# Kernel optimization log

Measured on AMD Instinct MI355X. Metric: run time of the kernel, lower is better.

The kernel has to match this reference:

```python
import jax, jax.numpy as jnp
import numpy as np
import math

N_HEAD = 32
ROPE_BASE = 10000.0


def _rope_headwise(x):
    # Faithful to the source bug: x is [B, H, S, D] and the rotary module uses
    # x.shape[1] (= H) as the "sequence length", so the angle depends on the
    # head index, broadcast over the true sequence axis.
    B, H, S, D = x.shape
    inv_freq = 1.0 / (ROPE_BASE ** (jnp.arange(0, D, 2, dtype=jnp.float32) / D))  # [D/2]
    t = jnp.arange(H, dtype=jnp.float32)                                          # [H]
    freqs = t[:, None] * inv_freq[None, :]                                        # [H, D/2]
    # emb = cat(freqs, freqs)[..., :D//2] == freqs, so cos/sin are just over freqs
    cos = jnp.cos(freqs)[None, :, None, :]   # [1, H, 1, D/2]
    sin = jnp.sin(freqs)[None, :, None, :]
    x1, x2 = x[..., : D // 2], x[..., D // 2 :]
    return jnp.concatenate([x1 * cos - x2 * sin, x1 * sin + x2 * cos], axis=-1)


def setup_inputs() -> dict:
    key = jax.random.key(0)
    ks = jax.random.split(key, 5)
    B, S, E = 2, 2048, 2048
    scale = 0.02
    return {
        "x": jax.random.normal(ks[0], (B, S, E), dtype=jnp.float32),
        "Wq": jax.random.normal(ks[1], (E, E), dtype=jnp.float32) * scale,
        "bq": jnp.zeros((E,), dtype=jnp.float32),
        "Wk": jax.random.normal(ks[2], (E, E), dtype=jnp.float32) * scale,
        "bk": jnp.zeros((E,), dtype=jnp.float32),
        "Wv": jax.random.normal(ks[3], (E, E), dtype=jnp.float32) * scale,
        "bv": jnp.zeros((E,), dtype=jnp.float32),
        "Wo": jax.random.normal(ks[4], (E, E), dtype=jnp.float32) * scale,
        "bo": jnp.zeros((E,), dtype=jnp.float32),
    }


def reference(x, Wq, bq, Wk, bk, Wv, bv, Wo, bo):
    B, S, E = x.shape
    H = N_HEAD
    D = E // H

    def split_heads(y):  # [B,S,E] -> [B,H,S,D]
        return y.reshape(B, S, H, D).transpose(0, 2, 1, 3)

    q = split_heads(x @ Wq + bq)
    k = split_heads(x @ Wk + bk)
    v = split_heads(x @ Wv + bv)

    q = _rope_headwise(q)
    k = _rope_headwise(k)

    scores = jnp.einsum("bhqd,bhkd->bhqk", q, k) / math.sqrt(D)  # [B,H,S,S]
    causal = jnp.triu(jnp.ones((S, S), dtype=bool), k=1)
    scores = jnp.where(causal[None, None], -jnp.inf, scores)
    attn = jax.nn.softmax(scores, axis=-1)
    out = jnp.einsum("bhqk,bhkd->bhqd", attn, v)                 # [B,H,S,D]
    out = out.transpose(0, 2, 1, 3).reshape(B, S, E)
    return out @ Wo + bo
```

## Files before the change

kernel.cpp:

```cpp
#include <hip/hip_runtime.h>
#include <hip/hip_bf16.h>

#define B_ 2
#define S_ 2048
#define E_ 2048
#define H_ 32
#define M_ (B_*S_)

typedef __bf16 bf16x8 __attribute__((ext_vector_type(8)));
typedef float  f32x4  __attribute__((ext_vector_type(4)));

__device__ __forceinline__ ushort f2bf(float f) {
    uint u = __float_as_uint(f);
    u += 0x7fffu + ((u >> 16) & 1u);
    return (ushort)(u >> 16);
}
__device__ __forceinline__ uint pack2bf(float a, float b) {
    __hip_bfloat162 h = __float22bfloat162_rn(make_float2(a, b));
    return *(uint*)&h;
}
__device__ __forceinline__ float bf2f(ushort h) {
    return __uint_as_float(((uint)h) << 16);
}
__device__ __forceinline__ f32x4 f4zero() {
    f32x4 z; z[0]=0.f; z[1]=0.f; z[2]=0.f; z[3]=0.f; return z;
}
__device__ __forceinline__ void async16(const ushort* g, ushort* l) {
    __builtin_amdgcn_global_load_lds((const __attribute__((address_space(1))) void*)g,
                                     (__attribute__((address_space(3))) void*)l, 16, 0, 0);
}

__global__ __launch_bounds__(256) void cast_x_kernel(const float* __restrict__ x,
                                                     ushort* __restrict__ xb) {
    int i = (blockIdx.x * 256 + threadIdx.x) * 4;
    float4 v = *(const float4*)(x + i);
    uint2 o;
    o.x = pack2bf(v.x, v.y);
    o.y = pack2bf(v.z, v.w);
    *(uint2*)(xb + i) = o;
}

__global__ __launch_bounds__(256) void wtrans_kernel(const float* __restrict__ W0, const float* __restrict__ W1,
                                                     const float* __restrict__ W2, const float* __restrict__ W3,
                                                     ushort* __restrict__ T0, ushort* __restrict__ T1,
                                                     ushort* __restrict__ T2, ushort* __restrict__ T3) {
    const float* W = (blockIdx.z==0)?W0:(blockIdx.z==1)?W1:(blockIdx.z==2)?W2:W3;
    ushort*      T = (blockIdx.z==0)?T0:(blockIdx.z==1)?T1:(blockIdx.z==2)?T2:T3;
    __shared__ float tile[64][65];
    const int k0 = blockIdx.y * 64, n0 = blockIdx.x * 64;
    const int rr = threadIdx.x >> 4;
    const int cc = (threadIdx.x & 15) * 4;
    #pragma unroll
    for (int p = 0; p < 4; ++p) {
        int r = p * 16 + rr;
        float4 v = *(const float4*)(W + (size_t)(k0 + r) * E_ + n0 + cc);
        tile[r][cc+0] = v.x; tile[r][cc+1] = v.y; tile[r][cc+2] = v.z; tile[r][cc+3] = v.w;
    }
    __syncthreads();
    #pragma unroll
    for (int p = 0; p < 4; ++p) {
        int rn = p * 16 + rr;
        uint2 o;
        o.x = pack2bf(tile[cc+0][rn], tile[cc+1][rn]);
        o.y = pack2bf(tile[cc+2][rn], tile[cc+3][rn]);
        *(uint2*)(T + (size_t)(n0 + rn) * E_ + k0 + cc) = o;
    }
}

__global__ __launch_bounds__(256) void vtrans_kernel(const ushort* __restrict__ vb,
                                                     ushort* __restrict__ vt) {
    __shared__ ushort tile[64][65];
    const int bh = blockIdx.y, b = bh >> 5, h = bh & 31;
    const int s0 = blockIdx.x * 64;
    int tx = threadIdx.x & 63, ty = threadIdx.x >> 6;
    #pragma unroll
    for (int it = 0; it < 16; ++it) {
        int r = it * 4 + ty;
        tile[r][tx] = vb[(size_t)(b * S_ + s0 + r) * E_ + h * 64 + tx];
    }
    __syncthreads();
    #pragma unroll
    for (int it = 0; it < 16; ++it) {
        int r = it * 4 + ty;
        vt[(size_t)(bh * 64 + r) * S_ + s0 + tx] = tile[tx][r];
    }
}

#define VMW4 asm volatile("s_waitcnt vmcnt(4)" ::: "memory")
#define VMW0 asm volatile("s_waitcnt vmcnt(0)" ::: "memory")
#define MEMB asm volatile("" ::: "memory")

#define STA_(bf, kt, h) { _Pragma("unroll") for (int it_ = 0; it_ < 2; ++it_) { \
    async16(A + (size_t)(m0 + it_*128 + (h)*64 + srow) * E_ + (kt)*64 + scg*8,  \
            &As[bf][(it_*128 + (h)*64 + wave*8) * 64]); } }

#define STB_(bf, kt, h) { _Pragma("unroll") for (int it_ = 0; it_ < 2; ++it_) { \
    int rih_ = it_*64 + srow;                                                   \
    int ldr_ = ((rih_ >> 5) << 6) + (h)*32 + (rih_ & 31);                       \
    int rwb_ = it_*64 + wave*8;                                                 \
    int wbs_ = ((rwb_ >> 5) << 6) + (h)*32 + (rwb_ & 31);                       \
    async16(Bt + (size_t)(n0 + ldr_) * E_ + (kt)*64 + scg*8,                    \
            &Bs[bf][wbs_ * 64]); } }

#define PHASE_(bf, mh, nh, LA, LB, STAGES) {                                    \
    if (LA) {                                                                   \
      _Pragma("unroll") for (int m_ = 0; m_ < 4; ++m_)                          \
        _Pragma("unroll") for (int k_ = 0; k_ < 2; ++k_) {                      \
          int row_ = wm*128 + ((mh)*4 + m_)*16 + l15;                           \
          pa[m_][k_] = *(const bf16x8*)(&As[bf][row_*64 + (((k_*4 + quad) ^ (row_ & 7)) << 3)]); } } \
    if (LB) {                                                                   \
      _Pragma("unroll") for (int n_ = 0; n_ < 2; ++n_)                          \
        _Pragma("unroll") for (int k_ = 0; k_ < 2; ++k_) {                      \
          int row_ = wn*64 + ((nh)*2 + n_)*16 + l15;                            \
          pb[n_][k_] = *(const bf16x8*)(&Bs[bf][row_*64 + (((k_*4 + quad) ^ (row_ & 7)) << 3)]); } } \
    STAGES;                                                                     \
    MEMB; __builtin_amdgcn_s_barrier();                                         \
    __builtin_amdgcn_s_setprio(1);                                              \
    _Pragma("unroll") for (int k_ = 0; k_ < 2; ++k_)                            \
      _Pragma("unroll") for (int m_ = 0; m_ < 4; ++m_)                          \
        _Pragma("unroll") for (int n_ = 0; n_ < 2; ++n_)                        \
          acc[(mh)*4+m_][(nh)*2+n_] = __builtin_amdgcn_mfma_f32_16x16x32_bf16(  \
              pa[m_][k_], pb[n_][k_], acc[(mh)*4+m_][(nh)*2+n_], 0, 0, 0);      \
    __builtin_amdgcn_s_setprio(0);                                              \
    asm volatile("s_waitcnt lgkmcnt(0)" ::: "memory");                          \
    __builtin_amdgcn_sched_barrier(0);                                          \
    MEMB; __builtin_amdgcn_s_barrier(); MEMB;                                   \
  }

template<bool OUTF32, bool DOROPE, int NZ>
__global__ __launch_bounds__(512, 2) void gemm256(const ushort* __restrict__ A,
        const ushort* __restrict__ Bt0, const ushort* __restrict__ Bt1, const ushort* __restrict__ Bt2,
        const float* __restrict__ bias0, const float* __restrict__ bias1, const float* __restrict__ bias2,
        void* __restrict__ C0, void* __restrict__ C1, void* __restrict__ C2) {
    const int bid = blockIdx.x;
    const int z   = bid % NZ;
    const int nb  = (bid / NZ) % (E_ / 256);
    const int mb  = bid / (NZ * (E_ / 256));

    const ushort* Bt  = (z==0)?Bt0:(z==1)?Bt1:Bt2;
    const float* bias = (z==0)?bias0:(z==1)?bias1:bias2;
    void* Cv          = (z==0)?C0:(z==1)?C1:C2;

    __shared__ ushort As[2][256 * 64];
    __shared__ ushort Bs[2][256 * 64];

    const int tid  = threadIdx.x;
    const int wave = tid >> 6, lane = tid & 63;
    const int quad = lane >> 4, l15 = lane & 15;
    const int wm = wave >> 2, wn = wave & 3;
    const int m0 = mb * 256, n0 = nb * 256;
    const int srow = tid >> 3;
    const int scg  = (tid & 7) ^ (srow & 7);

    f32x4 acc[8][4];
    #pragma unroll
    for (int i = 0; i < 8; ++i)
        #pragma unroll
        for (int j = 0; j < 4; ++j) acc[i][j] = f4zero();

    bf16x8 pa[4][2], pb[2][2];

    STA_(0, 0, 0); STA_(0, 0, 1); STB_(0, 0, 0); STB_(0, 0, 1);
    STA_(1, 1, 0); STB_(1, 1, 0);
    VMW4;
    MEMB; __builtin_amdgcn_s_barrier(); MEMB;

    #pragma unroll 1
    for (int i = 0; i < 15; ++i) {
        const int t1 = 2*i + 1, t2 = 2*i + 2, t3 = 2*i + 3;
        PHASE_(0, 0, 1, 1, 1, STB_(1, t1, 1));
        PHASE_(0, 0, 0, 0, 1, STA_(1, t1, 1));
        PHASE_(0, 1, 0, 1, 0, STA_(0, t2, 0));
        PHASE_(0, 1, 1, 0, 1, STB_(0, t2, 0); VMW4);
        PHASE_(1, 0, 1, 1, 1, STB_(0, t2, 1));
        PHASE_(1, 0, 0, 0, 1, STA_(0, t2, 1));
        PHASE_(1, 1, 0, 1, 0, STA_(1, t3, 0));
        PHASE_(1, 1, 1, 0, 1, STB_(1, t3, 0); VMW4);
    }
    PHASE_(0, 0, 1, 1, 1, STB_(1, 31, 1));
    PHASE_(0, 0, 0, 0, 1, STA_(1, 31, 1));
    PHASE_(0, 1, 0, 1, 0, {});
    PHASE_(0, 1, 1, 0, 1, VMW0);
    PHASE_(1, 0, 1, 1, 1, {});
    PHASE_(1, 0, 0, 0, 1, {});
    PHASE_(1, 1, 0, 1, 0, {});
    PHASE_(1, 1, 1, 0, 1, {});

    if (DOROPE && z != 2) {
        const float qsc = (z == 0) ? 0.125f * 1.44269504f : 1.0f;
        const int h = (n0 + wn * 64) >> 6;
        float sn[2], cs[2];
        #pragma unroll
        for (int nt = 0; nt < 2; ++nt) {
            int j = nt * 16 + l15;
            float ang = (float)h * __expf(-(float)j * 0.28782313662425575f);
            __sincosf(ang, &sn[nt], &cs[nt]);
        }
        ushort* C = (ushort*)Cv;
        #pragma unroll
        for (int f = 0; f < 8; ++f) {
            #pragma unroll
            for (int nt = 0; nt < 2; ++nt) {
                int col1 = n0 + wn * 64 + nt * 16 + l15;
                float b1 = bias[col1], b2 = bias[col1 + 32];
                #pragma unroll
                for (int r = 0; r < 4; ++r) {
                    int rowg = m0 + wm * 128 + f * 16 + quad * 4 + r;
                    float x1 = acc[f][nt][r] + b1;
                    float x2 = acc[f][nt + 2][r] + b2;
                    C[(size_t)rowg * E_ + col1]      = f2bf((x1 * cs[nt] - x2 * sn[nt]) * qsc);
                    C[(size_t)rowg * E_ + col1 + 32] = f2bf((x1 * sn[nt] + x2 * cs[nt]) * qsc);
                }
            }
        }
    } else {
        #pragma unroll
        for (int f = 0; f < 8; ++f) {
            #pragma unroll
            for (int nt = 0; nt < 4; ++nt) {
                int col = n0 + wn * 64 + nt * 16 + l15;
                float bv = bias[col];
                #pragma unroll
                for (int r = 0; r < 4; ++r) {
                    int rowg = m0 + wm * 128 + f * 16 + quad * 4 + r;
                    float v = acc[f][nt][r] + bv;
                    if (OUTF32) ((float*)Cv)[(size_t)rowg * E_ + col] = v;
                    else        ((ushort*)Cv)[(size_t)rowg * E_ + col] = f2bf(v);
                }
            }
        }
    }
}
#undef STA_
#undef STB_
#undef PHASE_

template<bool OUTF32, bool DOROPE, int NZ>
__global__ __launch_bounds__(256) void gemm128(const ushort* __restrict__ A,
        const ushort* __restrict__ Bt0, const ushort* __restrict__ Bt1, const ushort* __restrict__ Bt2,
        const float* __restrict__ bias0, const float* __restrict__ bias1, const float* __restrict__ bias2,
        void* __restrict__ C0, void* __restrict__ C1, void* __restrict__ C2) {
    const int bid = blockIdx.x;
    const int z   = bid % NZ;
    const int nb  = (bid / NZ) % (E_ / 128);
    const int mb  = bid / (NZ * (E_ / 128));

    const ushort* Bt  = (z==0)?Bt0:(z==1)?Bt1:Bt2;
    const float* bias = (z==0)?bias0:(z==1)?bias1:bias2;
    void* Cv          = (z==0)?C0:(z==1)?C1:C2;

    __shared__ ushort As[128 * 64];
    __shared__ ushort Bs[128 * 64];

    const int tid  = threadIdx.x;
    const int wave = tid >> 6, lane = tid & 63;
    const int quad = lane >> 4, l15 = lane & 15;
    const int wm = wave >> 1, wn = wave & 1;
    const int m0 = mb * 128, n0 = nb * 128;
    const int srow = tid >> 3;
    const int scgx = (tid & 7) ^ (srow & 7);

    f32x4 acc[4][4];
    #pragma unroll
    for (int i = 0; i < 4; ++i)
        #pragma unroll
        for (int j = 0; j < 4; ++j) acc[i][j] = f4zero();

    for (int k0 = 0; k0 < E_; k0 += 64) {
        #pragma unroll
        for (int it = 0; it < 4; ++it) {
            int r = it * 32 + srow;
            async16(A  + (size_t)(m0 + r) * E_ + k0 + scgx * 8, As + (it * 256 + wave * 64) * 8);
            async16(Bt + (size_t)(n0 + r) * E_ + k0 + scgx * 8, Bs + (it * 256 + wave * 64) * 8);
        }
        __syncthreads();
        #pragma unroll
        for (int kk = 0; kk < 2; ++kk) {
            bf16x8 af[4], bfr[4];
            #pragma unroll
            for (int mt = 0; mt < 4; ++mt) {
                int row = wm * 64 + mt * 16 + l15;
                af[mt] = *(const bf16x8*)(As + row * 64 + (((kk * 4 + quad) ^ (row & 7)) << 3));
            }
            #pragma unroll
            for (int nt = 0; nt < 4; ++nt) {
                int row = wn * 64 + nt * 16 + l15;
                bfr[nt] = *(const bf16x8*)(Bs + row * 64 + (((kk * 4 + quad) ^ (row & 7)) << 3));
            }
            #pragma unroll
            for (int mt = 0; mt < 4; ++mt)
                #pragma unroll
                for (int nt = 0; nt < 4; ++nt)
                    acc[mt][nt] = __builtin_amdgcn_mfma_f32_16x16x32_bf16(af[mt], bfr[nt], acc[mt][nt], 0, 0, 0);
        }
        __syncthreads();
    }

    if (DOROPE && z != 2) {
        const float qsc = (z == 0) ? 0.125f * 1.44269504f : 1.0f;
        const int h = (n0 + wn * 64) >> 6;
        float sn[2], cs[2];
        #pragma unroll
        for (int nt = 0; nt < 2; ++nt) {
            int j = nt * 16 + l15;
            float ang = (float)h * __expf(-(float)j * 0.28782313662425575f);
            __sincosf(ang, &sn[nt], &cs[nt]);
        }
        ushort* C = (ushort*)Cv;
        #pragma unroll
        for (int mt = 0; mt < 4; ++mt) {
            #pragma unroll
            for (int nt = 0; nt < 2; ++nt) {
                int col1 = n0 + wn * 64 + nt * 16 + l15;
                float b1 = bias[col1], b2 = bias[col1 + 32];
                #pragma unroll
                for (int r = 0; r < 4; ++r) {
                    int rowg = m0 + wm * 64 + mt * 16 + quad * 4 + r;
                    float x1 = acc[mt][nt][r] + b1;
                    float x2 = acc[mt][nt + 2][r] + b2;
                    C[(size_t)rowg * E_ + col1]      = f2bf((x1 * cs[nt] - x2 * sn[nt]) * qsc);
                    C[(size_t)rowg * E_ + col1 + 32] = f2bf((x1 * sn[nt] + x2 * cs[nt]) * qsc);
                }
            }
        }
    } else {
        #pragma unroll
        for (int mt = 0; mt < 4; ++mt) {
            #pragma unroll
            for (int nt = 0; nt < 4; ++nt) {
                int col = n0 + wn * 64 + nt * 16 + l15;
                float bv = bias[col];
                #pragma unroll
                for (int r = 0; r < 4; ++r) {
                    int rowg = m0 + wm * 64 + mt * 16 + quad * 4 + r;
                    float v = acc[mt][nt][r] + bv;
                    if (OUTF32) ((float*)Cv)[(size_t)rowg * E_ + col] = v;
                    else        ((ushort*)Cv)[(size_t)rowg * E_ + col] = f2bf(v);
                }
            }
        }
    }
}

__global__ __launch_bounds__(256) void flash_kernel(const ushort* __restrict__ qb,
        const ushort* __restrict__ kb, const ushort* __restrict__ vt,
        ushort* __restrict__ ctx) {
    __shared__ ushort KVs[2][2][64 * 64];
    __shared__ ushort Ps[4][32 * 64];

    const int tid  = threadIdx.x;
    const int wave = tid >> 6, lane = tid & 63;
    const int quad = lane >> 4, l15 = lane & 15;
    const int bh = blockIdx.y, b = bh >> 5, h = bh & 31;
    const int srow = tid >> 3;
    const int scgx = (tid & 7) ^ (srow & 7);
    ushort* Pw = Ps[wave];

    bf16x8 ones;
    #pragma unroll
    for (int j = 0; j < 8; ++j) ones[j] = (__bf16)1.0f;

    #pragma unroll 1
    for (int pass = 0; pass < 2; ++pass) {
        const int qx  = pass ? (15 - (int)blockIdx.x) : (int)blockIdx.x;
        const int q0  = qx * 128;
        const int qw0 = q0 + wave * 32;
        const int nkt = 2 * qx + 2;

        bf16x8 qf[2][2];
        #pragma unroll
        for (int mt = 0; mt < 2; ++mt)
            #pragma unroll
            for (int kk = 0; kk < 2; ++kk)
                qf[mt][kk] = *(const bf16x8*)(qb + (size_t)(b * S_ + qw0 + mt * 16 + l15) * E_ + h * 64 + kk * 32 + quad * 8);

        f32x4 oacc[2][4], lacc[2];
        #pragma unroll
        for (int mt = 0; mt < 2; ++mt) {
            lacc[mt] = f4zero();
            #pragma unroll
            for (int dt = 0; dt < 4; ++dt) oacc[mt][dt] = f4zero();
        }

        #pragma unroll
        for (int it = 0; it < 2; ++it) {
            int r = it * 32 + srow;
            async16(kb + (size_t)(b * S_ + r) * E_ + h * 64 + scgx * 8, KVs[0][0] + (it * 256 + wave * 64) * 8);
            async16(vt + (size_t)(bh * 64 + r) * S_ + scgx * 8,         KVs[0][1] + (it * 256 + wave * 64) * 8);
        }
        __syncthreads();

        #pragma unroll 1
        for (int kt = 0; kt < nkt; ++kt) {
            const int k0 = kt * 64;
            if (kt + 1 < nkt) {
                const int kn = k0 + 64;
                ushort* Kd = KVs[(kt + 1) & 1][0];
                ushort* Vd = KVs[(kt + 1) & 1][1];
                #pragma unroll
                for (int it = 0; it < 2; ++it) {
                    int r = it * 32 + srow;
                    async16(kb + (size_t)(b * S_ + kn + r) * E_ + h * 64 + scgx * 8, Kd + (it * 256 + wave * 64) * 8);
                    async16(vt + (size_t)(bh * 64 + r) * S_ + kn + scgx * 8,         Vd + (it * 256 + wave * 64) * 8);
                }
            }

            if (k0 <= qw0 + 31) {
                const ushort* Ks = KVs[kt & 1][0];
                const ushort* Vs = KVs[kt & 1][1];
                f32x4 sacc[2][4];
                #pragma unroll
                for (int mt = 0; mt < 2; ++mt)
                    #pragma unroll
                    for (int nt = 0; nt < 4; ++nt) sacc[mt][nt] = f4zero();
                #pragma unroll
                for (int kk = 0; kk < 2; ++kk)
                    #pragma unroll
                    for (int nt = 0; nt < 4; ++nt) {
                        int row = nt * 16 + l15;
                        bf16x8 kf = *(const bf16x8*)(Ks + row * 64 + (((kk * 4 + quad) ^ (row & 7)) << 3));
                        #pragma unroll
                        for (int mt = 0; mt < 2; ++mt)
                            sacc[mt][nt] = __builtin_amdgcn_mfma_f32_16x16x32_bf16(kf, qf[mt][kk], sacc[mt][nt], 0, 0, 0);
                    }

                #pragma unroll
                for (int mt = 0; mt < 2; ++mt) {
                    const int q  = qw0 + mt * 16 + l15;
                    const bool dm = (k0 + 63 > qw0 + mt * 16);
                    const int ql = mt * 16 + l15, swz = ql & 7;
                    #pragma unroll
                    for (int nt = 0; nt < 4; ++nt) {
                        float p[4];
                        #pragma unroll
                        for (int r = 0; r < 4; ++r) {
                            int s = k0 + nt * 16 + quad * 4 + r;
                            p[r] = exp2f(sacc[mt][nt][r]);
                            if (dm && s > q) p[r] = 0.f;
                        }
                        uint2 pk;
                        pk.x = pack2bf(p[0], p[1]);
                        pk.y = pack2bf(p[2], p[3]);
                        *(uint2*)(Pw + ql * 64 + (((nt * 2 + (quad >> 1)) ^ swz) << 3) + (quad & 1) * 4) = pk;
                    }
                }

                #pragma unroll
                for (int kk = 0; kk < 2; ++kk) {
                    bf16x8 pf[2];
                    #pragma unroll
                    for (int mt = 0; mt < 2; ++mt) {
                        int ql = mt * 16 + l15;
                        pf[mt] = *(const bf16x8*)(Pw + ql * 64 + (((kk * 4 + quad) ^ (ql & 7)) << 3));
                    }
                    #pragma unroll
                    for (int mt = 0; mt < 2; ++mt)
                        lacc[mt] = __builtin_amdgcn_mfma_f32_16x16x32_bf16(pf[mt], ones, lacc[mt], 0, 0, 0);
                    #pragma unroll
                    for (int dt = 0; dt < 4; ++dt) {
                        int row = dt * 16 + l15;
                        bf16x8 vf = *(const bf16x8*)(Vs + row * 64 + (((kk * 4 + quad) ^ (row & 7)) << 3));
                        #pragma unroll
                        for (int mt = 0; mt < 2; ++mt)
                            oacc[mt][dt] = __builtin_amdgcn_mfma_f32_16x16x32_bf16(pf[mt], vf, oacc[mt][dt], 0, 0, 0);
                    }
                }
            }
            __syncthreads();
        }

        #pragma unroll
        for (int mt = 0; mt < 2; ++mt)
            #pragma unroll
            for (int r = 0; r < 4; ++r) {
                float inv = 1.0f / lacc[mt][r];
                #pragma unroll
                for (int dt = 0; dt < 4; ++dt)
                    ctx[(size_t)(b * S_ + qw0 + mt * 16 + quad * 4 + r) * E_ + h * 64 + dt * 16 + l15] =
                        f2bf(oacc[mt][dt][r] * inv);
            }
    }
}

extern "C" void kernel_launch(void* const* d_in, const int* in_sizes, int n_in,
                              void* d_out, int out_size, void* d_ws, size_t ws_size,
                              hipStream_t stream) {
    const float* x  = (const float*)d_in[0];
    const float* Wq = (const float*)d_in[1];
    const float* bq = (const float*)d_in[2];
    const float* Wk = (const float*)d_in[3];
    const float* bk = (const float*)d_in[4];
    const float* Wv = (const float*)d_in[5];
    const float* bv = (const float*)d_in[6];
    const float* Wo = (const float*)d_in[7];
    const float* bo = (const float*)d_in[8];
    float* out = (float*)d_out;

    ushort* p   = (ushort*)d_ws;
    ushort* xb  = p; p += (size_t)M_ * E_;
    ushort* wqt = p; p += (size_t)E_ * E_;
    ushort* wkt = p; p += (size_t)E_ * E_;
    ushort* wvt = p; p += (size_t)E_ * E_;
    ushort* wot = p; p += (size_t)E_ * E_;
    ushort* qb  = p; p += (size_t)M_ * E_;
    ushort* kb  = p; p += (size_t)M_ * E_;
    ushort* vb  = p; p += (size_t)M_ * E_;
    ushort* ctx = p; p += (size_t)M_ * E_;
    ushort* vt  = xb;

    cast_x_kernel<<<(M_ * E_) / 1024, 256, 0, stream>>>(x, xb);
    wtrans_kernel<<<dim3(E_ / 64, E_ / 64, 4), 256, 0, stream>>>(Wq, Wk, Wv, Wo, wqt, wkt, wvt, wot);
    gemm256<false, true, 2><<<(E_ / 256) * (M_ / 256) * 2, 512, 0, stream>>>(
        xb, wqt, wkt, wkt, bq, bk, bk, qb, kb, kb);
    gemm128<false, false, 1><<<(E_ / 128) * (M_ / 128), 256, 0, stream>>>(
        xb, wvt, wvt, wvt, bv, bv, bv, vb, vb, vb);
    vtrans_kernel<<<dim3(S_ / 64, B_ * H_), 256, 0, stream>>>(vb, vt);
    flash_kernel<<<dim3(8, B_ * H_), 256, 0, stream>>>(qb, kb, vt, ctx);
    gemm128<true, false, 1><<<(E_ / 128) * (M_ / 128), 256, 0, stream>>>(
        ctx, wot, wot, wot, bo, bo, bo, out, out, out);
}
```

Before: 397.6 us.

## Split flash attention block into eight waves of 16 query rows each

The flash attention kernel moves from 4 waves each handling 32 query rows to 8 waves (512 threads) each handling 16 rows. That halves per-wave accumulator registers, doubles waves per block to hide latency, and lets each thread issue one K/V async load instead of two. It also adds a mask-free fast path for tiles entirely below the diagonal and uses the hardware exp2 builtin. The trade-off is less reuse of each K/V fragment read from LDS per MFMA, and a larger share of each block's time spent at barriers.

Measured after the change: 364.9 us. -8.2%, faster.

```diff
diff --git a/kernel.cpp b/kernel.cpp
--- a/kernel.cpp
+++ b/kernel.cpp
@@ -19,8 +19,12 @@
     __hip_bfloat162 h = __float22bfloat162_rn(make_float2(a, b));
     return *(uint*)&h;
 }
-__device__ __forceinline__ float bf2f(ushort h) {
-    return __uint_as_float(((uint)h) << 16);
+__device__ __forceinline__ float fexp2(float x) {
+#if __has_builtin(__builtin_amdgcn_exp2f)
+    return __builtin_amdgcn_exp2f(x);
+#else
+    return exp2f(x);
+#endif
 }
 __device__ __forceinline__ f32x4 f4zero() {
     f32x4 z; z[0]=0.f; z[1]=0.f; z[2]=0.f; z[3]=0.f; return z;
@@ -342,11 +346,11 @@
     }
 }
 
-__global__ __launch_bounds__(256) void flash_kernel(const ushort* __restrict__ qb,
+__global__ __launch_bounds__(512) void flash_kernel(const ushort* __restrict__ qb,
         const ushort* __restrict__ kb, const ushort* __restrict__ vt,
         ushort* __restrict__ ctx) {
     __shared__ ushort KVs[2][2][64 * 64];
-    __shared__ ushort Ps[4][32 * 64];
+    __shared__ ushort Ps[8][16 * 64];
 
     const int tid  = threadIdx.x;
     const int wave = tid >> 6, lane = tid & 63;
@@ -364,30 +368,20 @@
     for (int pass = 0; pass < 2; ++pass) {
         const int qx  = pass ? (15 - (int)blockIdx.x) : (int)blockIdx.x;
         const int q0  = qx * 128;
-        const int qw0 = q0 + wave * 32;
+        const int qw0 = q0 + wave * 16;
         const int nkt = 2 * qx + 2;
 
-        bf16x8 qf[2][2];
-        #pragma unroll
-        for (int mt = 0; mt < 2; ++mt)
-            #pragma unroll
-            for (int kk = 0; kk < 2; ++kk)
-                qf[mt][kk] = *(const bf16x8*)(qb + (size_t)(b * S_ + qw0 + mt * 16 + l15) * E_ + h * 64 + kk * 32 + quad * 8);
-
-        f32x4 oacc[2][4], lacc[2];
-        #pragma unroll
-        for (int mt = 0; mt < 2; ++mt) {
-            lacc[mt] = f4zero();
-            #pragma unroll
-            for (int dt = 0; dt < 4; ++dt) oacc[mt][dt] = f4zero();
-        }
-
-        #pragma unroll
-        for (int it = 0; it < 2; ++it) {
-            int r = it * 32 + srow;
-            async16(kb + (size_t)(b * S_ + r) * E_ + h * 64 + scgx * 8, KVs[0][0] + (it * 256 + wave * 64) * 8);
-            async16(vt + (size_t)(bh * 64 + r) * S_ + scgx * 8,         KVs[0][1] + (it * 256 + wave * 64) * 8);
-        }
+        bf16x8 qf[2];
+        #pragma unroll
+        for (int kk = 0; kk < 2; ++kk)
+            qf[kk] = *(const bf16x8*)(qb + (size_t)(b * S_ + qw0 + l15) * E_ + h * 64 + kk * 32 + quad * 8);
+
+        f32x4 oacc[4], lacc = f4zero();
+        #pragma unroll
+        for (int dt = 0; dt < 4; ++dt) oacc[dt] = f4zero();
+
+        async16(kb + (size_t)(b * S_ + srow) * E_ + h * 64 + scgx * 8, KVs[0][0] + wave * 512);
+        async16(vt + (size_t)(bh * 64 + srow) * S_ + scgx * 8,         KVs[0][1] + wave * 512);
         __syncthreads();
 
         #pragma unroll 1
@@ -395,74 +389,64 @@
             const int k0 = kt * 64;
             if (kt + 1 < nkt) {
                 const int kn = k0 + 64;
-                ushort* Kd = KVs[(kt + 1) & 1][0];
-                ushort* Vd = KVs[(kt + 1) & 1][1];
-                #pragma unroll
-                for (int it = 0; it < 2; ++it) {
-                    int r = it * 32 + srow;
-                    async16(kb + (size_t)(b * S_ + kn + r) * E_ + h * 64 + scgx * 8, Kd + (it * 256 + wave * 64) * 8);
-                    async16(vt + (size_t)(bh * 64 + r) * S_ + kn + scgx * 8,         Vd + (it * 256 + wave * 64) * 8);
-                }
-            }
-
-            if (k0 <= qw0 + 31) {
+                async16(kb + (size_t)(b * S_ + kn + srow) * E_ + h * 64 + scgx * 8,
+                        KVs[(kt + 1) & 1][0] + wave * 512);
+                async16(vt + (size_t)(bh * 64 + srow) * S_ + kn + scgx * 8,
+                        KVs[(kt + 1) & 1][1] + wave * 512);
+            }
+
+            if (k0 <= qw0 + 15) {
                 const ushort* Ks = KVs[kt & 1][0];
                 const ushort* Vs = KVs[kt & 1][1];
-                f32x4 sacc[2][4];
-                #pragma unroll
-                for (int mt = 0; mt < 2; ++mt)
-                    #pragma unroll
-                    for (int nt = 0; nt < 4; ++nt) sacc[mt][nt] = f4zero();
+                f32x4 sacc[4];
+                #pragma unroll
+                for (int nt = 0; nt < 4; ++nt) sacc[nt] = f4zero();
                 #pragma unroll
                 for (int kk = 0; kk < 2; ++kk)
                     #pragma unroll
                     for (int nt = 0; nt < 4; ++nt) {
                         int row = nt * 16 + l15;
                         bf16x8 kf = *(const bf16x8*)(Ks + row * 64 + (((kk * 4 + quad) ^ (row & 7)) << 3));
-                        #pragma unroll
-                        for (int mt = 0; mt < 2; ++mt)
-                            sacc[mt][nt] = __builtin_amdgcn_mfma_f32_16x16x32_bf16(kf, qf[mt][kk], sacc[mt][nt], 0, 0, 0);
+                        sacc[nt] = __builtin_amdgcn_mfma_f32_16x16x32_bf16(kf, qf[kk], sacc[nt], 0, 0, 0);
                     }
 
-                #pragma unroll
-                for (int mt = 0; mt < 2; ++mt) {
-                    const int q  = qw0 + mt * 16 + l15;
-                    const bool dm = (k0 + 63 > qw0 + mt * 16);
-                    const int ql = mt * 16 + l15, swz = ql & 7;
+                const bool dm = (k0 + 63 > qw0);
+                const int swz = l15 & 7;
+                if (dm) {
+                    const int q = qw0 + l15;
                     #pragma unroll
                     for (int nt = 0; nt < 4; ++nt) {
                         float p[4];
                         #pragma unroll
                         for (int r = 0; r < 4; ++r) {
                             int s = k0 + nt * 16 + quad * 4 + r;
-                            p[r] = exp2f(sacc[mt][nt][r]);
-                            if (dm && s > q) p[r] = 0.f;
+                            float e = fexp2(sacc[nt][r]);
+                            p[r] = (s > q) ? 0.f : e;
                         }
                         uint2 pk;
                         pk.x = pack2bf(p[0], p[1]);
                         pk.y = pack2bf(p[2], p[3]);
-                        *(uint2*)(Pw + ql * 64 + (((nt * 2 + (quad >> 1)) ^ swz) << 3) + (quad & 1) * 4) = pk;
+                        *(uint2*)(Pw + l15 * 64 + (((nt * 2 + (quad >> 1)) ^ swz) << 3) + (quad & 1) * 4) = pk;
+                    }
+                } else {
+                    #pragma unroll
+                    for (int nt = 0; nt < 4; ++nt) {
+                        uint2 pk;
+                        pk.x = pack2bf(fexp2(sacc[nt][0]), fexp2(sacc[nt][1]));
+                        pk.y = pack2bf(fexp2(sacc[nt][2]), fexp2(sacc[nt][3]));
+                        *(uint2*)(Pw + l15 * 64 + (((nt * 2 + (quad >> 1)) ^ swz) << 3) + (quad & 1) * 4) = pk;
                     }
                 }
 
                 #pragma unroll
                 for (int kk = 0; kk < 2; ++kk) {
-                    bf16x8 pf[2];
-                    #pragma unroll
-                    for (int mt = 0; mt < 2; ++mt) {
-                        int ql = mt * 16 + l15;
-                        pf[mt] = *(const bf16x8*)(Pw + ql * 64 + (((kk * 4 + quad) ^ (ql & 7)) << 3));
-                    }
-                    #pragma unroll
-                    for (int mt = 0; mt < 2; ++mt)
-                        lacc[mt] = __builtin_amdgcn_mfma_f32_16x16x32_bf16(pf[mt], ones, lacc[mt], 0, 0, 0);
+                    bf16x8 pf = *(const bf16x8*)(Pw + l15 * 64 + (((kk * 4 + quad) ^ swz) << 3));
+                    lacc = __builtin_amdgcn_mfma_f32_16x16x32_bf16(pf, ones, lacc, 0, 0, 0);
                     #pragma unroll
                     for (int dt = 0; dt < 4; ++dt) {
                         int row = dt * 16 + l15;
                         bf16x8 vf = *(const bf16x8*)(Vs + row * 64 + (((kk * 4 + quad) ^ (row & 7)) << 3));
-                        #pragma unroll
-                        for (int mt = 0; mt < 2; ++mt)
-                            oacc[mt][dt] = __builtin_amdgcn_mfma_f32_16x16x32_bf16(pf[mt], vf, oacc[mt][dt], 0, 0, 0);
+                        oacc[dt] = __builtin_amdgcn_mfma_f32_16x16x32_bf16(pf, vf, oacc[dt], 0, 0, 0);
                     }
                 }
             }
@@ -470,15 +454,13 @@
         }
 
         #pragma unroll
-        for (int mt = 0; mt < 2; ++mt)
-            #pragma unroll
-            for (int r = 0; r < 4; ++r) {
-                float inv = 1.0f / lacc[mt][r];
-                #pragma unroll
-                for (int dt = 0; dt < 4; ++dt)
-                    ctx[(size_t)(b * S_ + qw0 + mt * 16 + quad * 4 + r) * E_ + h * 64 + dt * 16 + l15] =
-                        f2bf(oacc[mt][dt][r] * inv);
-            }
+        for (int r = 0; r < 4; ++r) {
+            float inv = 1.0f / lacc[r];
+            #pragma unroll
+            for (int dt = 0; dt < 4; ++dt)
+                ctx[(size_t)(b * S_ + qw0 + quad * 4 + r) * E_ + h * 64 + dt * 16 + l15] =
+                    f2bf(oacc[dt][r] * inv);
+        }
     }
 }
 
@@ -515,7 +497,7 @@
     gemm128<false, false, 1><<<(E_ / 128) * (M_ / 128), 256, 0, stream>>>(
         xb, wvt, wvt, wvt, bv, bv, bv, vb, vb, vb);
     vtrans_kernel<<<dim3(S_ / 64, B_ * H_), 256, 0, stream>>>(vb, vt);
-    flash_kernel<<<dim3(8, B_ * H_), 256, 0, stream>>>(qb, kb, vt, ctx);
+    flash_kernel<<<dim3(8, B_ * H_), 512, 0, stream>>>(qb, kb, vt, ctx);
     gemm128<true, false, 1><<<(E_ / 128) * (M_ / 128), 256, 0, stream>>>(
         ctx, wot, wot, wot, bo, bo, bo, out, out, out);
 }
```
